# Optimization experiments

Measured on AMD Instinct MI355X. Metric: run time of the kernel, lower is better.

The kernel has to match this reference:

```python
import jax, jax.numpy as jnp
import numpy as np

NUM_CLASSES = 9
B, H, W = 8, 768, 768


def setup_inputs() -> dict:
    key = jax.random.key(0)
    k1, k2 = jax.random.split(key)
    masks = jax.random.randint(k1, (B, H, W), 0, NUM_CLASSES, dtype=jnp.int32)
    outputs = jax.random.normal(k2, (B, NUM_CLASSES, H, W), dtype=jnp.float32)
    return {"masks": masks, "outputs": outputs}


def reference(masks, outputs):
    b, c, h, w = outputs.shape
    k = NUM_CLASSES
    eye = jnp.eye(k, dtype=outputs.dtype)
    smooth = eye * 0.9 + (1.0 - eye) * (0.1 / 8.0)  # [K, K] smoothed targets

    # Fused segment-mean over all pixels: segment id = batch*K + class label.
    feats = jnp.transpose(outputs, (0, 2, 3, 1)).reshape(b * h * w, c)  # [BHW, C]
    ids = (jnp.arange(b, dtype=jnp.int32)[:, None, None] * k + masks).reshape(-1)
    sums = jax.ops.segment_sum(feats, ids, num_segments=b * k).reshape(b, k, c)
    counts = jax.ops.segment_sum(
        jnp.ones((b * h * w,), outputs.dtype), ids, num_segments=b * k
    ).reshape(b, k)

    # torch.unique(mask)[1:] drops label 0 (background); mask absent classes.
    protos = sums[:, 1:, :] / jnp.maximum(counts[:, 1:, None], 1.0)  # [B, K-1, C]
    present = counts[:, 1:] > 0  # [B, K-1]

    logp = jax.nn.log_softmax(protos, axis=-1)  # [B, K-1, C]
    tgt = smooth[1:]  # [K-1, C] soft targets for classes 1..K-1
    per_proto = -jnp.sum(tgt[None, :, :] * logp, axis=-1)  # [B, K-1]

    n_present = jnp.maximum(jnp.sum(present).astype(outputs.dtype), 1.0)
    loss = jnp.sum(jnp.where(present, per_proto, 0.0)) / n_present
    return loss
```

## Files before the change

### kernel.cpp

```cpp
#include <hip/hip_runtime.h>
#include <hip/hip_bf16.h>
#include <math.h>

#define NB 8
#define NC 9
#define PIXELS (768*768)
#define BLOCK 256
#define PPT 24
#define CHUNK_PX (BLOCK * PPT)
#define NCHUNK (PIXELS / CHUNK_PX)
#define NITER (PPT / 4)
#define NWAVE (BLOCK / 64)

#define SUMS_ELEMS (NB * 8 * NC)
#define WS_FLOATS (SUMS_ELEMS + NB * 8)

__global__ __launch_bounds__(BLOCK)
void accum_kernel(const int* __restrict__ masks,
                  const float* __restrict__ outputs,
                  float* __restrict__ sums,
                  float* __restrict__ counts)
{
    int blk = blockIdx.x;
    int chunk = blk % NCHUNK;
    int b = blk / NCHUNK;
    int t = threadIdx.x;
    int wave = t >> 6;
    int lane = t & 63;

    const int4* __restrict__ m4 =
        (const int4*)(masks + (size_t)b * PIXELS + (size_t)chunk * CHUNK_PX);
    int4 m[NITER];
    #pragma unroll
    for (int i = 0; i < NITER; ++i) m[i] = m4[t + i * BLOCK];

    __shared__ float red[NC][NWAVE][8];
    __shared__ float red_c[NWAVE][8];

    {
        int cnt[8];
        #pragma unroll
        for (int k = 0; k < 8; ++k) cnt[k] = 0;
        #pragma unroll
        for (int i = 0; i < NITER; ++i) {
            #pragma unroll
            for (int k = 1; k <= 8; ++k) {
                cnt[k - 1] += __popcll(__ballot(m[i].x == k));
                cnt[k - 1] += __popcll(__ballot(m[i].y == k));
                cnt[k - 1] += __popcll(__ballot(m[i].z == k));
                cnt[k - 1] += __popcll(__ballot(m[i].w == k));
            }
        }
        if (lane == 0) {
            #pragma unroll
            for (int k = 0; k < 8; ++k) red_c[wave][k] = (float)cnt[k];
        }
    }

    const float* outbase = outputs + (size_t)b * NC * PIXELS + (size_t)chunk * CHUNK_PX;

    float4 buf[NITER];
    {
        const float4* o4 = (const float4*)(outbase);
        #pragma unroll
        for (int i = 0; i < NITER; ++i) buf[i] = o4[t + i * BLOCK];
    }

    const int p = lane & 1;
    const int q = (lane >> 1) & 1;
    const int r = (lane >> 2) & 1;

    #pragma unroll
    for (int c = 0; c < NC; ++c) {
        float4 nxt[NITER];
        if (c < NC - 1) {
            const float4* o4 = (const float4*)(outbase + (size_t)(c + 1) * PIXELS);
            #pragma unroll
            for (int i = 0; i < NITER; ++i) nxt[i] = o4[t + i * BLOCK];
        }

        float s[8];
        #pragma unroll
        for (int k = 0; k < 8; ++k) s[k] = 0.f;

        #pragma unroll
        for (int i = 0; i < NITER; ++i) {
            float4 v = buf[i];
            #pragma unroll
            for (int k = 1; k <= 8; ++k) {
                float a = s[k - 1];
                a += (m[i].x == k) ? v.x : 0.f;
                a += (m[i].y == k) ? v.y : 0.f;
                a += (m[i].z == k) ? v.z : 0.f;
                a += (m[i].w == k) ? v.w : 0.f;
                s[k - 1] = a;
            }
        }

        float u[4];
        #pragma unroll
        for (int j = 0; j < 4; ++j) {
            float x = p ? s[j] : s[j + 4];
            float y = __shfl_xor(x, 1, 64);
            u[j] = (p ? s[j + 4] : s[j]) + y;
        }
        float v2[2];
        #pragma unroll
        for (int j = 0; j < 2; ++j) {
            float x = q ? u[j] : u[j + 2];
            float y = __shfl_xor(x, 2, 64);
            v2[j] = (q ? u[j + 2] : u[j]) + y;
        }
        float w;
        {
            float x = r ? v2[0] : v2[1];
            float y = __shfl_xor(x, 4, 64);
            w = (r ? v2[1] : v2[0]) + y;
        }
        w += __shfl_xor(w, 8, 64);
        w += __shfl_xor(w, 16, 64);
        w += __shfl_xor(w, 32, 64);

        if (lane < 8) {
            int cls = (p << 2) | (q << 1) | r;
            red[c][wave][cls] = w;
        }

        #pragma unroll
        for (int i = 0; i < NITER; ++i) buf[i] = nxt[i];
    }

    __syncthreads();

    if (t < NC * 8) {
        int c = t >> 3;
        int k = t & 7;
        float tot = 0.f;
        #pragma unroll
        for (int w = 0; w < NWAVE; ++w) tot += red[c][w][k];
        atomicAdd(&sums[(b * 8 + k) * NC + c], tot);
    } else if (t < NC * 8 + 8) {
        int k = t - NC * 8;
        float tot = 0.f;
        #pragma unroll
        for (int w = 0; w < NWAVE; ++w) tot += red_c[w][k];
        atomicAdd(&counts[b * 8 + k], tot);
    }
}

__global__ __launch_bounds__(64)
void finalize_kernel(const float* __restrict__ sums,
                     const float* __restrict__ counts,
                     float* __restrict__ out)
{
    int t = threadIdx.x;
    int b = t >> 3;
    int cls = t & 7;

    float cntv = counts[b * 8 + cls];
    float denom = fmaxf(cntv, 1.0f);

    float p[NC];
    float mx = -INFINITY;
    #pragma unroll
    for (int c = 0; c < NC; ++c) {
        p[c] = sums[(b * 8 + cls) * NC + c] / denom;
        mx = fmaxf(mx, p[c]);
    }
    float se = 0.f;
    #pragma unroll
    for (int c = 0; c < NC; ++c) se += expf(p[c] - mx);
    float lse = logf(se);

    float per = 0.f;
    #pragma unroll
    for (int c = 0; c < NC; ++c) {
        float tgt = (c == cls + 1) ? 0.9f : 0.0125f;
        per -= tgt * (p[c] - mx - lse);
    }

    bool present = cntv > 0.f;
    float val = present ? per : 0.f;
    float np  = present ? 1.f : 0.f;
    #pragma unroll
    for (int off = 32; off > 0; off >>= 1) {
        val += __shfl_down(val, off, 64);
        np  += __shfl_down(np,  off, 64);
    }
    if (t == 0) out[0] = val / fmaxf(np, 1.f);
}

extern "C" void kernel_launch(void* const* d_in, const int* in_sizes, int n_in,
                              void* d_out, int out_size, void* d_ws, size_t ws_size,
                              hipStream_t stream) {
    const int*   masks   = (const int*)d_in[0];
    const float* outputs = (const float*)d_in[1];
    float* sums   = (float*)d_ws;
    float* counts = sums + SUMS_ELEMS;

    hipMemsetAsync(d_ws, 0, WS_FLOATS * sizeof(float), stream);

    int grid = NB * NCHUNK;
    accum_kernel<<<grid, BLOCK, 0, stream>>>(masks, outputs, sums, counts);
    finalize_kernel<<<1, 64, 0, stream>>>(sums, counts, (float*)d_out);
}
```

Before: 260.3 us.

## Replace atomics with per-block partials, halve pixels per thread, drop prefetch

Each block now writes its per-class sums and counts to its own slot in a partials buffer instead of issuing atomicAdds. The finalize kernel reduces those partials with 640 threads before computing the loss, which also removes the workspace memset launch. Pixels per thread drop from 24 to 12, doubling the grid to raise memory-level parallelism. The software double-buffered prefetch of the next channel is replaced by a plain load per channel. In exchange, the finalize reduction becomes a serial pass over 192 partials per column on a single block.

```diff
diff --git a/kernel.cpp b/kernel.cpp
--- a/kernel.cpp
+++ b/kernel.cpp
@@ -6,20 +6,18 @@
 #define NC 9
 #define PIXELS (768*768)
 #define BLOCK 256
-#define PPT 24
+#define PPT 12
 #define CHUNK_PX (BLOCK * PPT)
 #define NCHUNK (PIXELS / CHUNK_PX)
 #define NITER (PPT / 4)
 #define NWAVE (BLOCK / 64)
-
-#define SUMS_ELEMS (NB * 8 * NC)
-#define WS_FLOATS (SUMS_ELEMS + NB * 8)
+#define GRID (NB * NCHUNK)
+#define SLOT 80
 
 __global__ __launch_bounds__(BLOCK)
 void accum_kernel(const int* __restrict__ masks,
                   const float* __restrict__ outputs,
-                  float* __restrict__ sums,
-                  float* __restrict__ counts)
+                  float* __restrict__ partial)
 {
     int blk = blockIdx.x;
     int chunk = blk % NCHUNK;
@@ -59,25 +57,16 @@
 
     const float* outbase = outputs + (size_t)b * NC * PIXELS + (size_t)chunk * CHUNK_PX;
 
-    float4 buf[NITER];
-    {
-        const float4* o4 = (const float4*)(outbase);
-        #pragma unroll
-        for (int i = 0; i < NITER; ++i) buf[i] = o4[t + i * BLOCK];
-    }
-
     const int p = lane & 1;
     const int q = (lane >> 1) & 1;
     const int r = (lane >> 2) & 1;
 
     #pragma unroll
     for (int c = 0; c < NC; ++c) {
-        float4 nxt[NITER];
-        if (c < NC - 1) {
-            const float4* o4 = (const float4*)(outbase + (size_t)(c + 1) * PIXELS);
-            #pragma unroll
-            for (int i = 0; i < NITER; ++i) nxt[i] = o4[t + i * BLOCK];
-        }
+        const float4* o4 = (const float4*)(outbase + (size_t)c * PIXELS);
+        float4 buf[NITER];
+        #pragma unroll
+        for (int i = 0; i < NITER; ++i) buf[i] = o4[t + i * BLOCK];
 
         float s[8];
         #pragma unroll
@@ -125,9 +114,6 @@
             int cls = (p << 2) | (q << 1) | r;
             red[c][wave][cls] = w;
         }
-
-        #pragma unroll
-        for (int i = 0; i < NITER; ++i) buf[i] = nxt[i];
     }
 
     __syncthreads();
@@ -138,56 +124,70 @@
         float tot = 0.f;
         #pragma unroll
         for (int w = 0; w < NWAVE; ++w) tot += red[c][w][k];
-        atomicAdd(&sums[(b * 8 + k) * NC + c], tot);
+        partial[(size_t)blk * SLOT + c * 8 + k] = tot;
     } else if (t < NC * 8 + 8) {
         int k = t - NC * 8;
         float tot = 0.f;
         #pragma unroll
         for (int w = 0; w < NWAVE; ++w) tot += red_c[w][k];
-        atomicAdd(&counts[b * 8 + k], tot);
+        partial[(size_t)blk * SLOT + 72 + k] = tot;
     }
 }
 
-__global__ __launch_bounds__(64)
-void finalize_kernel(const float* __restrict__ sums,
-                     const float* __restrict__ counts,
+__global__ __launch_bounds__(1024)
+void finalize_kernel(const float* __restrict__ partial,
                      float* __restrict__ out)
 {
+    __shared__ float tot[NB][SLOT];
     int t = threadIdx.x;
-    int b = t >> 3;
-    int cls = t & 7;
-
-    float cntv = counts[b * 8 + cls];
-    float denom = fmaxf(cntv, 1.0f);
-
-    float p[NC];
-    float mx = -INFINITY;
-    #pragma unroll
-    for (int c = 0; c < NC; ++c) {
-        p[c] = sums[(b * 8 + cls) * NC + c] / denom;
-        mx = fmaxf(mx, p[c]);
-    }
-    float se = 0.f;
-    #pragma unroll
-    for (int c = 0; c < NC; ++c) se += expf(p[c] - mx);
-    float lse = logf(se);
-
-    float per = 0.f;
-    #pragma unroll
-    for (int c = 0; c < NC; ++c) {
-        float tgt = (c == cls + 1) ? 0.9f : 0.0125f;
-        per -= tgt * (p[c] - mx - lse);
-    }
-
-    bool present = cntv > 0.f;
-    float val = present ? per : 0.f;
-    float np  = present ? 1.f : 0.f;
-    #pragma unroll
-    for (int off = 32; off > 0; off >>= 1) {
-        val += __shfl_down(val, off, 64);
-        np  += __shfl_down(np,  off, 64);
-    }
-    if (t == 0) out[0] = val / fmaxf(np, 1.f);
+
+    if (t < NB * SLOT) {
+        int b = t / SLOT;
+        int col = t % SLOT;
+        const float* p = partial + (size_t)b * NCHUNK * SLOT + col;
+        float s = 0.f;
+        #pragma unroll 8
+        for (int blk = 0; blk < NCHUNK; ++blk) s += p[(size_t)blk * SLOT];
+        tot[b][col] = s;
+    }
+    __syncthreads();
+
+    if (t < 64) {
+        int b = t >> 3;
+        int cls = t & 7;
+
+        float cntv = tot[b][72 + cls];
+        float denom = fmaxf(cntv, 1.0f);
+
+        float pr[NC];
+        float mx = -INFINITY;
+        #pragma unroll
+        for (int c = 0; c < NC; ++c) {
+            pr[c] = tot[b][c * 8 + cls] / denom;
+            mx = fmaxf(mx, pr[c]);
+        }
+        float se = 0.f;
+        #pragma unroll
+        for (int c = 0; c < NC; ++c) se += expf(pr[c] - mx);
+        float lse = logf(se);
+
+        float per = 0.f;
+        #pragma unroll
+        for (int c = 0; c < NC; ++c) {
+            float tgt = (c == cls + 1) ? 0.9f : 0.0125f;
+            per -= tgt * (pr[c] - mx - lse);
+        }
+
+        bool present = cntv > 0.f;
+        float val = present ? per : 0.f;
+        float np  = present ? 1.f : 0.f;
+        #pragma unroll
+        for (int off = 32; off > 0; off >>= 1) {
+            val += __shfl_down(val, off, 64);
+            np  += __shfl_down(np,  off, 64);
+        }
+        if (t == 0) out[0] = val / fmaxf(np, 1.f);
+    }
 }
 
 extern "C" void kernel_launch(void* const* d_in, const int* in_sizes, int n_in,
@@ -195,12 +195,8 @@
                               hipStream_t stream) {
     const int*   masks   = (const int*)d_in[0];
     const float* outputs = (const float*)d_in[1];
-    float* sums   = (float*)d_ws;
-    float* counts = sums + SUMS_ELEMS;
-
-    hipMemsetAsync(d_ws, 0, WS_FLOATS * sizeof(float), stream);
-
-    int grid = NB * NCHUNK;
-    accum_kernel<<<grid, BLOCK, 0, stream>>>(masks, outputs, sums, counts);
-    finalize_kernel<<<1, 64, 0, stream>>>(sums, counts, (float*)d_out);
+    float* partial = (float*)d_ws;
+
+    accum_kernel<<<GRID, BLOCK, 0, stream>>>(masks, outputs, partial);
+    finalize_kernel<<<1, 1024, 0, stream>>>(partial, (float*)d_out);
 }
```

After: 258.5 us. About the same (-0.7%).
